# Kernel optimization log

Measured on AMD Instinct MI355X. Metric: run time of the kernel, lower is better.

Reference implementation:

```python
import jax, jax.numpy as jnp
import numpy as np

N = 50000   # num_embs = num nodes
E = 800000  # num edges
D = 256     # feature dim
L = 4       # num layers
EPS = 1e-5


def setup_inputs() -> dict:
    key = jax.random.key(0)
    ks = jax.random.split(key, 8)
    scale = 1.0 / np.sqrt(D)
    return {
        "x": jax.random.normal(ks[0], (N, D), dtype=jnp.float32),  # ignored by forward
        "edge_index": jax.random.randint(ks[1], (2, E), 0, N, dtype=jnp.int32),
        "edge_weight": jax.random.uniform(ks[2], (E,), dtype=jnp.float32),
        "emb_weight": jax.random.normal(ks[3], (N, D), dtype=jnp.float32),
        "ln_w": jnp.ones((L, D), dtype=jnp.float32),
        "ln_b": jnp.zeros((L, D), dtype=jnp.float32),
        "conv_w": jax.random.normal(ks[4], (L, D, D), dtype=jnp.float32) * scale,
        "conv_b": jnp.zeros((L, D), dtype=jnp.float32),
        "post_w": jax.random.normal(ks[5], (D, D), dtype=jnp.float32) * scale,
        "post_b": jnp.zeros((D,), dtype=jnp.float32),
    }


def _layer_norm(h, w, b):
    mu = jnp.mean(h, axis=-1, keepdims=True)
    var = jnp.mean(jnp.square(h - mu), axis=-1, keepdims=True)
    return (h - mu) * jax.lax.rsqrt(var + EPS) * w + b


def reference(x, edge_index, edge_weight, emb_weight, ln_w, ln_b, conv_w, conv_b, post_w, post_b):
    # GCNConv semantics (PyG defaults): add self-loops (weight 1), symmetric norm.
    loop = jnp.arange(N, dtype=edge_index.dtype)
    src = jnp.concatenate([edge_index[0], loop])
    dst = jnp.concatenate([edge_index[1], loop])
    w = jnp.concatenate([edge_weight, jnp.ones((N,), edge_weight.dtype)])
    deg = jax.ops.segment_sum(w, dst, num_segments=N)
    dinv = jnp.where(deg > 0, jax.lax.rsqrt(jnp.maximum(deg, 1e-12)), 0.0)
    coef = (dinv[src] * w * dinv[dst])[:, None]  # [E+N, 1]

    h = emb_weight  # forward ignores x; cond_emb is None
    for i in range(L):
        z = _layer_norm(h, ln_w[i], ln_b[i])          # node LayerNorm
        zw = z @ conv_w[i]                             # linear transform
        agg = jax.ops.segment_sum(coef * zw[src], dst, num_segments=N)
        z = agg + conv_b[i]
        z = jax.nn.gelu(z, approximate=False)          # torch GELU is exact
        h = z + h                                      # residual (dropout=0)
    return h @ post_w + post_b
```

## Files before the change

### kernel.cpp

```cpp
#include <hip/hip_runtime.h>
#include <hip/hip_bf16.h>

#define N_NODES 50000
#define N_EDGES 800000
#define DIM     256
#define NLAYERS 4
#define EPS     1e-5f
#define SCAN_B  196
#define MASK40  ((1ULL << 40) - 1)
#define EPACK_CAP (N_EDGES + 7 * N_NODES + 16)

typedef __bf16 bf16x8 __attribute__((ext_vector_type(8)));
typedef float  f32x4  __attribute__((ext_vector_type(4)));
typedef unsigned short u16x8 __attribute__((ext_vector_type(8)));

__device__ __forceinline__ unsigned short f2b(float f) {
    __hip_bfloat16 h = __float2bfloat16(f);
    return __builtin_bit_cast(unsigned short, h);
}
__device__ __forceinline__ float b2f(unsigned short u) {
    unsigned int v = ((unsigned int)u) << 16;
    return __builtin_bit_cast(float, v);
}
__device__ __forceinline__ float gelu_exact(float x) {
    return 0.5f * x * (1.0f + erff(x * 0.70710678118654752f));
}

__global__ __launch_bounds__(256) void hist_kernel(const int* __restrict__ dst,
                                                   const float* __restrict__ w,
                                                   unsigned long long* __restrict__ cnt64,
                                                   int* __restrict__ rank) {
    int e = blockIdx.x * 256 + threadIdx.x;
    if (e >= N_EDGES) return;
    int d = dst[e];
    unsigned long long wfix = (unsigned long long)(w[e] * 4294967296.0f);
    unsigned long long old = atomicAdd(&cnt64[d], (1ULL << 40) | wfix);
    rank[e] = (int)(old >> 40);
}

__global__ __launch_bounds__(256) void scan_a_kernel(const unsigned long long* __restrict__ cnt64,
                                                     float* __restrict__ dinv,
                                                     int* __restrict__ bsum) {
    __shared__ int l[256];
    int i = blockIdx.x * 256 + threadIdx.x;
    int pc = 0;
    if (i < N_NODES) {
        unsigned long long v = cnt64[i];
        int cnt = (int)(v >> 40);
        float sw = (float)(v & MASK40) * 2.3283064365386963e-10f;
        dinv[i] = rsqrtf(1.0f + sw);
        pc = (cnt + 7) & ~7;
    }
    l[threadIdx.x] = pc;
    __syncthreads();
    for (int o = 128; o > 0; o >>= 1) {
        if (threadIdx.x < o) l[threadIdx.x] += l[threadIdx.x + o];
        __syncthreads();
    }
    if (threadIdx.x == 0) bsum[blockIdx.x] = l[0];
}

__global__ __launch_bounds__(256) void scan_b_kernel(const int* __restrict__ bsum,
                                                     int* __restrict__ boff,
                                                     int* __restrict__ rowptr) {
    __shared__ int l[256];
    int t = threadIdx.x;
    l[t] = (t < SCAN_B) ? bsum[t] : 0;
    __syncthreads();
    if (t == 0) {
        int run = 0;
        for (int j = 0; j < SCAN_B; ++j) { int v = l[j]; l[j] = run; run += v; }
        rowptr[N_NODES] = run;
    }
    __syncthreads();
    boff[t] = l[t];
}

__global__ __launch_bounds__(256) void scan_c_kernel(const unsigned long long* __restrict__ cnt64,
                                                     const int* __restrict__ boff,
                                                     int* __restrict__ rowptr) {
    __shared__ int l[256];
    int i = blockIdx.x * 256 + threadIdx.x;
    int pc = 0;
    if (i < N_NODES) {
        int cnt = (int)(cnt64[i] >> 40);
        pc = (cnt + 7) & ~7;
    }
    l[threadIdx.x] = pc;
    __syncthreads();
    if (threadIdx.x == 0) {
        int run = 0;
        for (int j = 0; j < 256; ++j) { int v = l[j]; l[j] = run; run += v; }
    }
    __syncthreads();
    if (i < N_NODES) rowptr[i] = boff[blockIdx.x] + l[threadIdx.x];
}

__global__ __launch_bounds__(256) void fill_kernel(const int* __restrict__ src,
                                                   const int* __restrict__ dst,
                                                   const float* __restrict__ w,
                                                   const float* __restrict__ dinv,
                                                   const int* __restrict__ rowptr,
                                                   const int* __restrict__ rank,
                                                   int2* __restrict__ epack) {
    int e = blockIdx.x * 256 + threadIdx.x;
    if (e >= N_EDGES) return;
    int s = src[e], d = dst[e];
    float c = dinv[s] * w[e] * dinv[d];
    int p = rowptr[d] + rank[e];
    epack[p] = make_int2(s << 9, __float_as_int(c));
}

__global__ __launch_bounds__(256) void convw_kernel(const float* __restrict__ conv_w,
                                                    const float* __restrict__ post_w,
                                                    unsigned short* __restrict__ Wt) {
    int idx = blockIdx.x * 256 + threadIdx.x;
    if (idx >= 5 * 65536) return;
    int m = idx >> 16;
    int r = idx & 65535;
    int n = r >> 8;
    int k = r & 255;
    float v = (m < 4) ? conv_w[m * 65536 + k * 256 + n] : post_w[k * 256 + n];
    Wt[idx] = f2b(v);
}

__global__ __launch_bounds__(256) void ln_cast_kernel(const float* __restrict__ H,
                                                      const float* __restrict__ lnw,
                                                      const float* __restrict__ lnb,
                                                      unsigned short* __restrict__ Z) {
    int row = blockIdx.x * 4 + (threadIdx.x >> 6);
    int lane = threadIdx.x & 63;
    const float4 x = *(const float4*)(H + (size_t)row * DIM + lane * 4);
    float s = x.x + x.y + x.z + x.w;
    for (int o = 32; o > 0; o >>= 1) s += __shfl_xor(s, o);
    float mu = s * (1.0f / DIM);
    float d0 = x.x - mu, d1 = x.y - mu, d2 = x.z - mu, d3 = x.w - mu;
    float v = d0 * d0 + d1 * d1 + d2 * d2 + d3 * d3;
    for (int o = 32; o > 0; o >>= 1) v += __shfl_xor(v, o);
    float rs = rsqrtf(v * (1.0f / DIM) + EPS);
    const float4 ww = *(const float4*)(lnw + lane * 4);
    const float4 bb = *(const float4*)(lnb + lane * 4);
    ushort4 o4;
    o4.x = f2b(d0 * rs * ww.x + bb.x);
    o4.y = f2b(d1 * rs * ww.y + bb.y);
    o4.z = f2b(d2 * rs * ww.z + bb.z);
    o4.w = f2b(d3 * rs * ww.w + bb.w);
    *(ushort4*)(Z + (size_t)row * DIM + lane * 4) = o4;
}

template <int MODE>
__device__ __forceinline__ void gemm_body(const unsigned short* __restrict__ A,
                                          const unsigned short* __restrict__ Bt,
                                          void* __restrict__ Cout,
                                          const float* __restrict__ bias) {
    int tid = threadIdx.x;
    int wave = tid >> 6;
    int lane = tid & 63;
    int q = lane >> 4;
    int c16 = lane & 15;
    int mbase = blockIdx.x * 64;
    int cbase = wave * 64;

    const unsigned short* aptr[4];
    #pragma unroll
    for (int nt = 0; nt < 4; ++nt) {
        int row = mbase + nt * 16 + c16;
        if (row >= N_NODES) row = N_NODES - 1;
        aptr[nt] = A + (size_t)row * DIM;
    }
    const unsigned short* wptr[4];
    #pragma unroll
    for (int ct = 0; ct < 4; ++ct)
        wptr[ct] = Bt + (size_t)(cbase + ct * 16 + c16) * DIM;

    f32x4 acc[4][4] = {};
    #pragma unroll 1
    for (int k0 = 0; k0 < DIM; k0 += 32) {
        bf16x8 nf[4], wf[4];
        #pragma unroll
        for (int nt = 0; nt < 4; ++nt)
            nf[nt] = __builtin_bit_cast(bf16x8, *(const u16x8*)(aptr[nt] + k0 + q * 8));
        #pragma unroll
        for (int ct = 0; ct < 4; ++ct)
            wf[ct] = __builtin_bit_cast(bf16x8, *(const u16x8*)(wptr[ct] + k0 + q * 8));
        #pragma unroll
        for (int nt = 0; nt < 4; ++nt)
            #pragma unroll
            for (int ct = 0; ct < 4; ++ct)
                acc[nt][ct] = __builtin_amdgcn_mfma_f32_16x16x32_bf16(wf[ct], nf[nt], acc[nt][ct], 0, 0, 0);
    }

    float4 bb[4];
    if (MODE == 1) {
        #pragma unroll
        for (int ct = 0; ct < 4; ++ct)
            bb[ct] = *(const float4*)(bias + cbase + ct * 16 + q * 4);
    }
    #pragma unroll
    for (int nt = 0; nt < 4; ++nt) {
        int node = mbase + nt * 16 + c16;
        if (node >= N_NODES) continue;
        #pragma unroll
        for (int ct = 0; ct < 4; ++ct) {
            int chan = cbase + ct * 16 + q * 4;
            if (MODE == 0) {
                unsigned short* C = (unsigned short*)Cout;
                ushort4 o4;
                o4.x = f2b(acc[nt][ct][0]);
                o4.y = f2b(acc[nt][ct][1]);
                o4.z = f2b(acc[nt][ct][2]);
                o4.w = f2b(acc[nt][ct][3]);
                *(ushort4*)(C + (size_t)node * DIM + chan) = o4;
            } else {
                float* C = (float*)Cout;
                float4 o;
                o.x = acc[nt][ct][0] + bb[ct].x;
                o.y = acc[nt][ct][1] + bb[ct].y;
                o.z = acc[nt][ct][2] + bb[ct].z;
                o.w = acc[nt][ct][3] + bb[ct].w;
                *(float4*)(C + (size_t)node * DIM + chan) = o;
            }
        }
    }
}

__global__ __launch_bounds__(256) void gemm_bf16_kernel(const unsigned short* __restrict__ A,
                                                        const unsigned short* __restrict__ Bt,
                                                        unsigned short* __restrict__ C) {
    gemm_body<0>(A, Bt, C, nullptr);
}

__global__ __launch_bounds__(256) void gemm_f32_kernel(const unsigned short* __restrict__ A,
                                                       const unsigned short* __restrict__ Bt,
                                                       float* __restrict__ C,
                                                       const float* __restrict__ bias) {
    gemm_body<1>(A, Bt, C, bias);
}

__global__ __launch_bounds__(256) void agg_kernel(const char* __restrict__ ZW,
                                                  const float* __restrict__ Hin,
                                                  float* __restrict__ Hout,
                                                  const float* __restrict__ bias,
                                                  const int* __restrict__ rowptr,
                                                  const int2* __restrict__ epack,
                                                  const float* __restrict__ dinv,
                                                  const float* __restrict__ lnw,
                                                  const float* __restrict__ lnb,
                                                  unsigned short* __restrict__ Zout,
                                                  int doLN, int writeH) {
    int node = blockIdx.x * 4 + (threadIdx.x >> 6);
    int lane = threadIdx.x & 63;
    int g = lane >> 5;
    int colB = (lane & 31) * 16;

    float di = dinv[node];
    float scg = (g == 0) ? di * di : 0.0f;
    const u16x8 zs = *(const u16x8*)(ZW + node * 512 + colB);
    float a[8];
    #pragma unroll
    for (int j = 0; j < 8; ++j) a[j] = scg * b2f(zs[j]);

    int e0 = rowptr[node], e1 = rowptr[node + 1];
    for (int e = e0; e < e1; e += 8) {
        const int2* pp = epack + e + 4 * g;
        const int4 q0 = *(const int4*)pp;
        const int4 q1 = *(const int4*)(pp + 2);
        const u16x8 v0 = *(const u16x8*)(ZW + q0.x + colB);
        const u16x8 v1 = *(const u16x8*)(ZW + q0.z + colB);
        const u16x8 v2 = *(const u16x8*)(ZW + q1.x + colB);
        const u16x8 v3 = *(const u16x8*)(ZW + q1.z + colB);
        float c0 = __int_as_float(q0.y);
        float c1 = __int_as_float(q0.w);
        float c2 = __int_as_float(q1.y);
        float c3 = __int_as_float(q1.w);
        #pragma unroll
        for (int j = 0; j < 8; ++j) {
            a[j] += c0 * b2f(v0[j]);
            a[j] += c1 * b2f(v1[j]);
            a[j] += c2 * b2f(v2[j]);
            a[j] += c3 * b2f(v3[j]);
        }
    }
    #pragma unroll
    for (int j = 0; j < 8; ++j) a[j] += __shfl_xor(a[j], 32);

    int col0 = (lane & 31) * 8;
    const float4 bb0 = *(const float4*)(bias + col0);
    const float4 bb1 = *(const float4*)(bias + col0 + 4);
    const float4 h0 = *(const float4*)(Hin + (size_t)node * DIM + col0);
    const float4 h1 = *(const float4*)(Hin + (size_t)node * DIM + col0 + 4);
    float o[8];
    o[0] = h0.x + gelu_exact(a[0] + bb0.x);
    o[1] = h0.y + gelu_exact(a[1] + bb0.y);
    o[2] = h0.z + gelu_exact(a[2] + bb0.z);
    o[3] = h0.w + gelu_exact(a[3] + bb0.w);
    o[4] = h1.x + gelu_exact(a[4] + bb1.x);
    o[5] = h1.y + gelu_exact(a[5] + bb1.y);
    o[6] = h1.z + gelu_exact(a[6] + bb1.z);
    o[7] = h1.w + gelu_exact(a[7] + bb1.w);

    if (writeH && g == 0) {
        float4 w0, w1;
        w0.x = o[0]; w0.y = o[1]; w0.z = o[2]; w0.w = o[3];
        w1.x = o[4]; w1.y = o[5]; w1.z = o[6]; w1.w = o[7];
        *(float4*)(Hout + (size_t)node * DIM + col0) = w0;
        *(float4*)(Hout + (size_t)node * DIM + col0 + 4) = w1;
    }

    float y[8];
    #pragma unroll
    for (int j = 0; j < 8; ++j) y[j] = o[j];
    if (doLN) {
        float s = 0.0f;
        #pragma unroll
        for (int j = 0; j < 8; ++j) s += o[j];
        for (int off = 16; off > 0; off >>= 1) s += __shfl_xor(s, off);
        float mu = s * (1.0f / DIM);
        float v = 0.0f;
        float d[8];
        #pragma unroll
        for (int j = 0; j < 8; ++j) { d[j] = o[j] - mu; v += d[j] * d[j]; }
        for (int off = 16; off > 0; off >>= 1) v += __shfl_xor(v, off);
        float rs = rsqrtf(v * (1.0f / DIM) + EPS);
        const float4 ww0 = *(const float4*)(lnw + col0);
        const float4 ww1 = *(const float4*)(lnw + col0 + 4);
        const float4 lb0 = *(const float4*)(lnb + col0);
        const float4 lb1 = *(const float4*)(lnb + col0 + 4);
        y[0] = d[0] * rs * ww0.x + lb0.x;
        y[1] = d[1] * rs * ww0.y + lb0.y;
        y[2] = d[2] * rs * ww0.z + lb0.z;
        y[3] = d[3] * rs * ww0.w + lb0.w;
        y[4] = d[4] * rs * ww1.x + lb1.x;
        y[5] = d[5] * rs * ww1.y + lb1.y;
        y[6] = d[6] * rs * ww1.z + lb1.z;
        y[7] = d[7] * rs * ww1.w + lb1.w;
    }
    if (g == 0) {
        u16x8 z;
        #pragma unroll
        for (int j = 0; j < 8; ++j) z[j] = f2b(y[j]);
        *(u16x8*)(Zout + (size_t)node * DIM + col0) = z;
    }
}

extern "C" void kernel_launch(void* const* d_in, const int* in_sizes, int n_in,
                              void* d_out, int out_size, void* d_ws, size_t ws_size,
                              hipStream_t stream) {
    const int*   ei     = (const int*)d_in[1];
    const int*   src    = ei;
    const int*   dst    = ei + N_EDGES;
    const float* ew     = (const float*)d_in[2];
    const float* emb    = (const float*)d_in[3];
    const float* ln_w   = (const float*)d_in[4];
    const float* ln_b   = (const float*)d_in[5];
    const float* conv_w = (const float*)d_in[6];
    const float* conv_b = (const float*)d_in[7];
    const float* post_w = (const float*)d_in[8];
    const float* post_b = (const float*)d_in[9];
    float* out = (float*)d_out;

    char* w = (char*)d_ws;
    size_t off = 0;
    auto alloc = [&](size_t bytes) -> char* {
        char* p = w + off;
        off += (bytes + 255) & ~(size_t)255;
        return p;
    };
    unsigned long long* cnt64 = (unsigned long long*)alloc((size_t)N_NODES * 8);
    float* dinv   = (float*)alloc((size_t)N_NODES * 4);
    int*   rank   = (int*)alloc((size_t)N_EDGES * 4);
    int*   rowptr = (int*)alloc((size_t)(N_NODES + 1) * 4);
    int*   bsum   = (int*)alloc(256 * 4);
    int*   boff   = (int*)alloc(256 * 4);
    int2*  epack  = (int2*)alloc((size_t)EPACK_CAP * 8);
    unsigned short* Wt  = (unsigned short*)alloc((size_t)5 * 65536 * 2);
    unsigned short* Z16 = (unsigned short*)alloc((size_t)N_NODES * DIM * 2);
    unsigned short* ZWb = (unsigned short*)alloc((size_t)N_NODES * DIM * 2);
    float* H  = (float*)alloc((size_t)N_NODES * DIM * 4);

    hipMemsetAsync(cnt64, 0, (size_t)N_NODES * 8, stream);
    hipMemsetAsync(epack, 0, (size_t)EPACK_CAP * 8, stream);
    hist_kernel<<<N_EDGES / 256, 256, 0, stream>>>(dst, ew, cnt64, rank);
    scan_a_kernel<<<SCAN_B, 256, 0, stream>>>(cnt64, dinv, bsum);
    scan_b_kernel<<<1, 256, 0, stream>>>(bsum, boff, rowptr);
    scan_c_kernel<<<SCAN_B, 256, 0, stream>>>(cnt64, boff, rowptr);
    fill_kernel<<<N_EDGES / 256, 256, 0, stream>>>(src, dst, ew, dinv, rowptr, rank, epack);
    convw_kernel<<<(5 * 65536) / 256, 256, 0, stream>>>(conv_w, post_w, Wt);

    const int GEMM_GRID = (N_NODES + 63) / 64;
    ln_cast_kernel<<<N_NODES / 4, 256, 0, stream>>>(emb, ln_w, ln_b, Z16);
    const float* hin = emb;
    for (int l = 0; l < NLAYERS; ++l) {
        gemm_bf16_kernel<<<GEMM_GRID, 256, 0, stream>>>(Z16, Wt + (size_t)l * 65536, ZWb);
        int doLN = (l < NLAYERS - 1) ? 1 : 0;
        int writeH = (l < NLAYERS - 1) ? 1 : 0;
        const float* nlw = doLN ? (ln_w + (l + 1) * DIM) : nullptr;
        const float* nlb = doLN ? (ln_b + (l + 1) * DIM) : nullptr;
        agg_kernel<<<N_NODES / 4, 256, 0, stream>>>((const char*)ZWb, hin, H, conv_b + l * DIM,
                                                    rowptr, epack, dinv, nlw, nlb,
                                                    Z16, doLN, writeH);
        hin = H;
    }
    gemm_f32_kernel<<<GEMM_GRID, 256, 0, stream>>>(Z16, Wt + (size_t)4 * 65536, out, post_b);
}
```

Before: 682.2 us.

## Store residual in bf16, widen edge padding to 16, unroll GEMM k-loop

The residual stream H is now kept in bf16 instead of fp32, which halves its read and write traffic in the aggregation kernel. The ln_cast kernel produces the initial bf16 copy. Edge rows are padded to multiples of 16 so each half-wave issues 8 gathers per iteration instead of 4, raising memory-level parallelism at the cost of more padding entries. The GEMM k-loop is unrolled by 2. Rounding the residual to bf16 at every layer compounds error across the 4 layers.

```diff
diff --git a/kernel.cpp b/kernel.cpp
--- a/kernel.cpp
+++ b/kernel.cpp
@@ -8,7 +8,7 @@
 #define EPS     1e-5f
 #define SCAN_B  196
 #define MASK40  ((1ULL << 40) - 1)
-#define EPACK_CAP (N_EDGES + 7 * N_NODES + 16)
+#define EPACK_CAP (N_EDGES + 15 * N_NODES + 32)
 
 typedef __bf16 bf16x8 __attribute__((ext_vector_type(8)));
 typedef float  f32x4  __attribute__((ext_vector_type(4)));
@@ -49,7 +49,7 @@
         int cnt = (int)(v >> 40);
         float sw = (float)(v & MASK40) * 2.3283064365386963e-10f;
         dinv[i] = rsqrtf(1.0f + sw);
-        pc = (cnt + 7) & ~7;
+        pc = (cnt + 15) & ~15;
     }
     l[threadIdx.x] = pc;
     __syncthreads();
@@ -84,7 +84,7 @@
     int pc = 0;
     if (i < N_NODES) {
         int cnt = (int)(cnt64[i] >> 40);
-        pc = (cnt + 7) & ~7;
+        pc = (cnt + 15) & ~15;
     }
     l[threadIdx.x] = pc;
     __syncthreads();
@@ -127,7 +127,8 @@
 __global__ __launch_bounds__(256) void ln_cast_kernel(const float* __restrict__ H,
                                                       const float* __restrict__ lnw,
                                                       const float* __restrict__ lnb,
-                                                      unsigned short* __restrict__ Z) {
+                                                      unsigned short* __restrict__ Z,
+                                                      unsigned short* __restrict__ Hbf) {
     int row = blockIdx.x * 4 + (threadIdx.x >> 6);
     int lane = threadIdx.x & 63;
     const float4 x = *(const float4*)(H + (size_t)row * DIM + lane * 4);
@@ -146,6 +147,9 @@
     o4.z = f2b(d2 * rs * ww.z + bb.z);
     o4.w = f2b(d3 * rs * ww.w + bb.w);
     *(ushort4*)(Z + (size_t)row * DIM + lane * 4) = o4;
+    ushort4 h4;
+    h4.x = f2b(x.x); h4.y = f2b(x.y); h4.z = f2b(x.z); h4.w = f2b(x.w);
+    *(ushort4*)(Hbf + (size_t)row * DIM + lane * 4) = h4;
 }
 
 template <int MODE>
@@ -174,7 +178,7 @@
         wptr[ct] = Bt + (size_t)(cbase + ct * 16 + c16) * DIM;
 
     f32x4 acc[4][4] = {};
-    #pragma unroll 1
+    #pragma unroll 2
     for (int k0 = 0; k0 < DIM; k0 += 32) {
         bf16x8 nf[4], wf[4];
         #pragma unroll
@@ -238,8 +242,7 @@
 }
 
 __global__ __launch_bounds__(256) void agg_kernel(const char* __restrict__ ZW,
-                                                  const float* __restrict__ Hin,
-                                                  float* __restrict__ Hout,
+                                                  unsigned short* __restrict__ Hbf,
                                                   const float* __restrict__ bias,
                                                   const int* __restrict__ rowptr,
                                                   const int2* __restrict__ epack,
@@ -261,24 +264,34 @@
     for (int j = 0; j < 8; ++j) a[j] = scg * b2f(zs[j]);
 
     int e0 = rowptr[node], e1 = rowptr[node + 1];
-    for (int e = e0; e < e1; e += 8) {
-        const int2* pp = epack + e + 4 * g;
+    for (int e = e0; e < e1; e += 16) {
+        const int2* pp = epack + e + 8 * g;
         const int4 q0 = *(const int4*)pp;
         const int4 q1 = *(const int4*)(pp + 2);
+        const int4 q2 = *(const int4*)(pp + 4);
+        const int4 q3 = *(const int4*)(pp + 6);
         const u16x8 v0 = *(const u16x8*)(ZW + q0.x + colB);
         const u16x8 v1 = *(const u16x8*)(ZW + q0.z + colB);
         const u16x8 v2 = *(const u16x8*)(ZW + q1.x + colB);
         const u16x8 v3 = *(const u16x8*)(ZW + q1.z + colB);
-        float c0 = __int_as_float(q0.y);
-        float c1 = __int_as_float(q0.w);
-        float c2 = __int_as_float(q1.y);
-        float c3 = __int_as_float(q1.w);
+        const u16x8 v4 = *(const u16x8*)(ZW + q2.x + colB);
+        const u16x8 v5 = *(const u16x8*)(ZW + q2.z + colB);
+        const u16x8 v6 = *(const u16x8*)(ZW + q3.x + colB);
+        const u16x8 v7 = *(const u16x8*)(ZW + q3.z + colB);
+        float c0 = __int_as_float(q0.y), c1 = __int_as_float(q0.w);
+        float c2 = __int_as_float(q1.y), c3 = __int_as_float(q1.w);
+        float c4 = __int_as_float(q2.y), c5 = __int_as_float(q2.w);
+        float c6 = __int_as_float(q3.y), c7 = __int_as_float(q3.w);
         #pragma unroll
         for (int j = 0; j < 8; ++j) {
             a[j] += c0 * b2f(v0[j]);
             a[j] += c1 * b2f(v1[j]);
             a[j] += c2 * b2f(v2[j]);
             a[j] += c3 * b2f(v3[j]);
+            a[j] += c4 * b2f(v4[j]);
+            a[j] += c5 * b2f(v5[j]);
+            a[j] += c6 * b2f(v6[j]);
+            a[j] += c7 * b2f(v7[j]);
         }
     }
     #pragma unroll
@@ -287,24 +300,22 @@
     int col0 = (lane & 31) * 8;
     const float4 bb0 = *(const float4*)(bias + col0);
     const float4 bb1 = *(const float4*)(bias + col0 + 4);
-    const float4 h0 = *(const float4*)(Hin + (size_t)node * DIM + col0);
-    const float4 h1 = *(const float4*)(Hin + (size_t)node * DIM + col0 + 4);
+    const u16x8 hv = *(const u16x8*)(Hbf + (size_t)node * DIM + col0);
     float o[8];
-    o[0] = h0.x + gelu_exact(a[0] + bb0.x);
-    o[1] = h0.y + gelu_exact(a[1] + bb0.y);
-    o[2] = h0.z + gelu_exact(a[2] + bb0.z);
-    o[3] = h0.w + gelu_exact(a[3] + bb0.w);
-    o[4] = h1.x + gelu_exact(a[4] + bb1.x);
-    o[5] = h1.y + gelu_exact(a[5] + bb1.y);
-    o[6] = h1.z + gelu_exact(a[6] + bb1.z);
-    o[7] = h1.w + gelu_exact(a[7] + bb1.w);
+    o[0] = b2f(hv[0]) + gelu_exact(a[0] + bb0.x);
+    o[1] = b2f(hv[1]) + gelu_exact(a[1] + bb0.y);
+    o[2] = b2f(hv[2]) + gelu_exact(a[2] + bb0.z);
+    o[3] = b2f(hv[3]) + gelu_exact(a[3] + bb0.w);
+    o[4] = b2f(hv[4]) + gelu_exact(a[4] + bb1.x);
+    o[5] = b2f(hv[5]) + gelu_exact(a[5] + bb1.y);
+    o[6] = b2f(hv[6]) + gelu_exact(a[6] + bb1.z);
+    o[7] = b2f(hv[7]) + gelu_exact(a[7] + bb1.w);
 
     if (writeH && g == 0) {
-        float4 w0, w1;
-        w0.x = o[0]; w0.y = o[1]; w0.z = o[2]; w0.w = o[3];
-        w1.x = o[4]; w1.y = o[5]; w1.z = o[6]; w1.w = o[7];
-        *(float4*)(Hout + (size_t)node * DIM + col0) = w0;
-        *(float4*)(Hout + (size_t)node * DIM + col0 + 4) = w1;
+        u16x8 hw;
+        #pragma unroll
+        for (int j = 0; j < 8; ++j) hw[j] = f2b(o[j]);
+        *(u16x8*)(Hbf + (size_t)node * DIM + col0) = hw;
     }
 
     float y[8];
@@ -376,7 +387,7 @@
     unsigned short* Wt  = (unsigned short*)alloc((size_t)5 * 65536 * 2);
     unsigned short* Z16 = (unsigned short*)alloc((size_t)N_NODES * DIM * 2);
     unsigned short* ZWb = (unsigned short*)alloc((size_t)N_NODES * DIM * 2);
-    float* H  = (float*)alloc((size_t)N_NODES * DIM * 4);
+    unsigned short* Hbf = (unsigned short*)alloc((size_t)N_NODES * DIM * 2);
 
     hipMemsetAsync(cnt64, 0, (size_t)N_NODES * 8, stream);
     hipMemsetAsync(epack, 0, (size_t)EPACK_CAP * 8, stream);
@@ -388,18 +399,16 @@
     convw_kernel<<<(5 * 65536) / 256, 256, 0, stream>>>(conv_w, post_w, Wt);
 
     const int GEMM_GRID = (N_NODES + 63) / 64;
-    ln_cast_kernel<<<N_NODES / 4, 256, 0, stream>>>(emb, ln_w, ln_b, Z16);
-    const float* hin = emb;
+    ln_cast_kernel<<<N_NODES / 4, 256, 0, stream>>>(emb, ln_w, ln_b, Z16, Hbf);
     for (int l = 0; l < NLAYERS; ++l) {
         gemm_bf16_kernel<<<GEMM_GRID, 256, 0, stream>>>(Z16, Wt + (size_t)l * 65536, ZWb);
         int doLN = (l < NLAYERS - 1) ? 1 : 0;
         int writeH = (l < NLAYERS - 1) ? 1 : 0;
         const float* nlw = doLN ? (ln_w + (l + 1) * DIM) : nullptr;
         const float* nlb = doLN ? (ln_b + (l + 1) * DIM) : nullptr;
-        agg_kernel<<<N_NODES / 4, 256, 0, stream>>>((const char*)ZWb, hin, H, conv_b + l * DIM,
+        agg_kernel<<<N_NODES / 4, 256, 0, stream>>>((const char*)ZWb, Hbf, conv_b + l * DIM,
                                                     rowptr, epack, dinv, nlw, nlb,
                                                     Z16, doLN, writeH);
-        hin = H;
     }
     gemm_f32_kernel<<<GEMM_GRID, 256, 0, stream>>>(Z16, Wt + (size_t)4 * 65536, out, post_b);
 }
```

Result: no change. 687.2 us (+0.7%).
